# Performance work log

Hardware: AMD Instinct MI355X
Metric: run time of the kernel (lower is better)

The kernel has to match this reference:

```python
import jax, jax.numpy as jnp
import numpy as np
from jax import lax

B_SZ, C_IN, C_OUT, H_IM, W_IM = 2, 128, 128, 64, 64
N_STATE = 16
DT_RANK = 4  # ceil(128/32)


def _ln_cf(x, w, b, eps=1e-6):
    # channels_first LayerNorm over channel dim
    u = x.mean(1, keepdims=True)
    s = ((x - u) ** 2).mean(1, keepdims=True)
    return w[None, :, None, None] * (x - u) / jnp.sqrt(s + eps) + b[None, :, None, None]


def _bn_train(x, g, b, eps=1e-5):
    # BatchNorm2d in training mode (batch statistics, biased variance)
    m = x.mean((0, 2, 3), keepdims=True)
    v = ((x - m) ** 2).mean((0, 2, 3), keepdims=True)
    return g[None, :, None, None] * (x - m) / jnp.sqrt(v + eps) + b[None, :, None, None]


def _dwconv(x, w, b):
    y = lax.conv_general_dilated(x, w, (1, 1), 'SAME', feature_group_count=x.shape[1],
                                 dimension_numbers=('NCHW', 'OIHW', 'NCHW'))
    return y + b[None, :, None, None]


def _conv1x1(x, w, b):
    return jnp.einsum('oi,bihw->bohw', w, x) + b[None, :, None, None]


def _selective_scan(u, dt, A, Bm, Cm, D, delta_bias):
    # u, dt: [B,Ch,L]; A: [Ch,N]; Bm, Cm: [B,N,L]; D: [Ch]
    dt = jax.nn.softplus(dt + delta_bias[None, :, None])
    xs = (dt.transpose(2, 0, 1), u.transpose(2, 0, 1), Bm.transpose(2, 0, 1), Cm.transpose(2, 0, 1))
    h0 = jnp.zeros(u.shape[:2] + (A.shape[1],), u.dtype)

    def step(h, inp):
        dt_t, u_t, b_t, c_t = inp
        dA = jnp.exp(dt_t[..., None] * A)                        # [B,Ch,N]
        h = h * dA + (dt_t * u_t)[..., None] * b_t[:, None, :]   # [B,Ch,N]
        return h, jnp.einsum('bcn,bn->bc', h, c_t)

    _, ys = lax.scan(step, h0, xs)
    return ys.transpose(1, 2, 0) + u * D[None, :, None]


def _ssm_apply(u, Wx, bx, Wdt, bdt, Alog, D, r):
    # u: [B,Ch,L]. Replicates torch row-major .reshape of [(B L),D] -> [B,D,L].
    Bb, Ch, L = u.shape
    N = Alog.shape[1]
    x_flat = u.transpose(0, 2, 1).reshape(Bb * L, Ch)   # 'b c l -> (b l) c'
    x_dbl = x_flat @ Wx.T + bx
    dt = (x_dbl[:, :r] @ Wdt.T + bdt).reshape(Bb, Wdt.shape[0], L)
    Bm = x_dbl[:, r:r + N].reshape(Bb, N, L)
    Cm = x_dbl[:, r + N:].reshape(Bb, N, L)
    return _selective_scan(u, dt, -jnp.exp(Alog), Bm, Cm, D, bdt)


def _forward(x, ln_in_w, ln_in_b, inproj_w, inproj_b, ln_mamba_w, ln_mamba_b, convm_w, convm_b,
             convr_w, convr_b, ln_cat_w, ln_cat_b, xproj_f_w, xproj_f_b, dtproj_f_w, dtproj_f_b,
             Alog_f, D_f, xproj_b_w, xproj_b_b, dtproj_b_w, dtproj_b_b, Alog_b, D_b,
             xproj_u_w, xproj_u_b, dtproj_u_w, dtproj_u_b, Alog_u, D_u, gate1_w, gate1_b,
             bn_g, bn_b, gate2_w, gate2_b, outproj_w, outproj_b, outln_w, outln_b):
    Bb, C, H, W = x.shape
    L = H * W
    half = C // 2
    x = _ln_cf(x, ln_in_w, ln_in_b)
    xp = _conv1x1(x, inproj_w, inproj_b)
    x_mamba, x_res = xp[:, :C], xp[:, C:]
    x_mamba = _ln_cf(x_mamba, ln_mamba_w, ln_mamba_b)
    x_mamba = jax.nn.silu(_dwconv(x_mamba, convm_w, convm_b))
    x_res = jax.nn.silu(_dwconv(x_res, convr_w, convr_b))
    # forward scan on first half of channels
    xf = x_mamba[:, :half].reshape(Bb, half, L)
    yf = _ssm_apply(xf, xproj_f_w, xproj_f_b, dtproj_f_w, dtproj_f_b, Alog_f, D_f, DT_RANK).reshape(Bb, half, H, W)
    # backward scan on second half (flip H,W, scan, flip back)
    xb = x_mamba[:, half:][:, :, ::-1, ::-1]
    yb = _ssm_apply(xb.reshape(Bb, half, L), xproj_b_w, xproj_b_b, dtproj_b_w, dtproj_b_b,
                    Alog_b, D_b, DT_RANK).reshape(Bb, half, H, W)[:, :, ::-1, ::-1]
    concat = _ln_cf(jnp.concatenate([yf, yb], axis=1), ln_cat_w, ln_cat_b)
    # uncertainty-ordered scan on full x_mamba
    sig = jax.nn.sigmoid(x_mamba.mean(1, keepdims=True))
    unc = (-(sig * jnp.log(sig + 1e-6))).reshape(Bb, L)
    idx = jnp.argsort(-unc, axis=1)       # descending uncertainty
    inv = jnp.argsort(idx, axis=1)        # inverse permutation
    xs = jnp.take_along_axis(x_mamba.reshape(Bb, C, L), idx[:, None, :], axis=2)
    yu = _ssm_apply(xs, xproj_u_w, xproj_u_b, dtproj_u_w, dtproj_u_b, Alog_u, D_u, 2 * DT_RANK)
    yu = jnp.take_along_axis(yu, inv[:, None, :], axis=2).reshape(Bb, C, H, W)
    # gated fusion
    g = jax.nn.relu(_bn_train(_conv1x1(jnp.concatenate([concat, yu], 1), gate1_w, gate1_b), bn_g, bn_b))
    g = jax.nn.sigmoid(_conv1x1(g, gate2_w, gate2_b))
    fused = g * yu + (1.0 - g) * concat
    out = _conv1x1(jnp.concatenate([fused, x_res], 1), outproj_w, outproj_b)
    return _ln_cf(out, outln_w, outln_b)


def setup_inputs() -> dict:
    key = jax.random.key(0)
    ks = jax.random.split(key, 16)
    C, half, R, N = C_IN, C_IN // 2, DT_RANK, N_STATE
    rn = lambda k, shp, s=0.02: jax.random.normal(k, shp, jnp.float32) * s

    def inv_dt(k, n):
        dt = jnp.exp(jax.random.uniform(k, (n,)) * (np.log(0.1) - np.log(0.001)) + np.log(0.001))
        dt = jnp.maximum(dt, 1e-4)
        return dt + jnp.log(-jnp.expm1(-dt))

    std = R ** -0.5
    Alog_h = jnp.log(jnp.broadcast_to(jnp.arange(1, N + 1, dtype=jnp.float32), (half, N)))
    Alog_fl = jnp.log(jnp.broadcast_to(jnp.arange(1, N + 1, dtype=jnp.float32), (C, N)))
    return {
        'x': jax.random.normal(ks[0], (B_SZ, C, H_IM, W_IM), jnp.float32),
        'ln_in_w': jnp.ones(C), 'ln_in_b': jnp.zeros(C),
        'inproj_w': rn(ks[1], (2 * C, C)), 'inproj_b': jnp.zeros(2 * C),
        'ln_mamba_w': jnp.ones(C), 'ln_mamba_b': jnp.zeros(C),
        'convm_w': rn(ks[2], (C, 1, 3, 3), 0.1), 'convm_b': jnp.zeros(C),
        'convr_w': rn(ks[3], (C, 1, 3, 3), 0.1), 'convr_b': jnp.zeros(C),
        'ln_cat_w': jnp.ones(C), 'ln_cat_b': jnp.zeros(C),
        'xproj_f_w': rn(ks[4], (R + 2 * N, half)), 'xproj_f_b': jnp.zeros(R + 2 * N),
        'dtproj_f_w': jax.random.uniform(ks[5], (half, R), minval=-std, maxval=std),
        'dtproj_f_b': inv_dt(ks[6], half),
        'Alog_f': Alog_h, 'D_f': jnp.ones(half),
        'xproj_b_w': rn(ks[7], (R + 2 * N, half)), 'xproj_b_b': jnp.zeros(R + 2 * N),
        'dtproj_b_w': jax.random.uniform(ks[8], (half, R), minval=-std, maxval=std),
        'dtproj_b_b': inv_dt(ks[9], half),
        'Alog_b': Alog_h, 'D_b': jnp.ones(half),
        'xproj_u_w': rn(ks[10], (2 * R + 2 * N, C)), 'xproj_u_b': jnp.zeros(2 * R + 2 * N),
        'dtproj_u_w': jax.random.uniform(ks[11], (C, 2 * R), minval=-std, maxval=std),
        'dtproj_u_b': inv_dt(ks[12], C),
        'Alog_u': Alog_fl, 'D_u': jnp.ones(C),
        'gate1_w': rn(ks[13], (C, 2 * C)), 'gate1_b': jnp.zeros(C),
        'bn_g': jnp.ones(C), 'bn_b': jnp.zeros(C),
        'gate2_w': rn(ks[14], (C, C)), 'gate2_b': jnp.zeros(C),
        'outproj_w': rn(ks[15], (C_OUT, 2 * C)), 'outproj_b': jnp.zeros(C_OUT),
        'outln_w': jnp.ones(C_OUT), 'outln_b': jnp.zeros(C_OUT),
    }


def reference(x, ln_in_w, ln_in_b, inproj_w, inproj_b, ln_mamba_w, ln_mamba_b, convm_w, convm_b,
              convr_w, convr_b, ln_cat_w, ln_cat_b, xproj_f_w, xproj_f_b, dtproj_f_w, dtproj_f_b,
              Alog_f, D_f, xproj_b_w, xproj_b_b, dtproj_b_w, dtproj_b_b, Alog_b, D_b,
              xproj_u_w, xproj_u_b, dtproj_u_w, dtproj_u_b, Alog_u, D_u, gate1_w, gate1_b,
              bn_g, bn_b, gate2_w, gate2_b, outproj_w, outproj_b, outln_w, outln_b):
    return _forward(x, ln_in_w, ln_in_b, inproj_w, inproj_b, ln_mamba_w, ln_mamba_b, convm_w, convm_b,
                    convr_w, convr_b, ln_cat_w, ln_cat_b, xproj_f_w, xproj_f_b, dtproj_f_w, dtproj_f_b,
                    Alog_f, D_f, xproj_b_w, xproj_b_b, dtproj_b_w, dtproj_b_b, Alog_b, D_b,
                    xproj_u_w, xproj_u_b, dtproj_u_w, dtproj_u_b, Alog_u, D_u, gate1_w, gate1_b,
                    bn_g, bn_b, gate2_w, gate2_b, outproj_w, outproj_b, outln_w, outln_b)
```

## Files before the change

### kernel.cpp

```cpp
#include <hip/hip_runtime.h>
#include <cstdint>
#include <cstddef>

#define TPB 256

namespace {

constexpr int B_SZ = 2;
constexpr int C    = 128;
constexpr int HALF = 64;
constexpr int L    = 4096;
constexpr int N    = 16;
constexpr int HH   = 64;
constexpr int WW   = 64;

__device__ __forceinline__ float softplusf(float x) {
  return fmaxf(x, 0.f) + __logf(1.f + __expf(-fabsf(x)));
}
__device__ __forceinline__ float sigm(float x) { return 1.f / (1.f + __expf(-x)); }

__device__ __forceinline__ unsigned long long unc_key(float u, int i) {
  unsigned m = __float_as_uint(u);
  m = (m & 0x80000000u) ? ~m : (m | 0x80000000u);
  return ((unsigned long long)(~m) << 32) | (unsigned)i;
}

__global__ void k_pixstats(const float* __restrict__ X, int bsX, int Cn, float eps,
                           float* __restrict__ mean, float* __restrict__ rinv) {
  const int lp = threadIdx.x & 63;
  const int wv = threadIdx.x >> 6;
  const int p  = blockIdx.x * 64 + lp;
  const int b = p / L, l = p % L;
  const int Cq = Cn >> 2;
  const float* Xp = X + (size_t)b * bsX + l;
  float s = 0.f, s2 = 0.f;
#pragma unroll 8
  for (int i = 0; i < Cq; ++i) {
    float v = Xp[(size_t)(wv * Cq + i) * L];
    s += v; s2 += v * v;
  }
  __shared__ float r1[4][64], r2[4][64];
  r1[wv][lp] = s; r2[wv][lp] = s2;
  __syncthreads();
  if (wv == 0) {
    float st  = r1[0][lp] + r1[1][lp] + r1[2][lp] + r1[3][lp];
    float s2t = r2[0][lp] + r2[1][lp] + r2[2][lp] + r2[3][lp];
    float m = st / Cn;
    float var = s2t / Cn - m * m;
    mean[p] = m;
    rinv[p] = rsqrtf(var + eps);
  }
}

template <int O_PB>
__global__ void k_conv_ln(const float* __restrict__ X, int bsX,
                          const float* __restrict__ lnw, const float* __restrict__ lnb,
                          const float* __restrict__ W, const float* __restrict__ bias,
                          float* __restrict__ Y, int I, int O) {
  __shared__ float Wl[O_PB * 128];
  __shared__ float aw[128], ab[128];
  const int o0 = blockIdx.y * O_PB;
  const int b  = blockIdx.z;
  for (int t = threadIdx.x; t < O_PB * I; t += TPB) {
    int i = t / O_PB, k = t % O_PB;
    Wl[t] = W[(size_t)(o0 + k) * I + i];
  }
  for (int t = threadIdx.x; t < I; t += TPB) { aw[t] = lnw[t]; ab[t] = lnb[t]; }
  __syncthreads();
  const int l0 = blockIdx.x * (2 * TPB) + threadIdx.x;
  const int l1 = l0 + TPB;
  const float* X0 = X + (size_t)b * bsX + l0;
  const float* X1 = X + (size_t)b * bsX + l1;
  float s0 = 0.f, q0 = 0.f, s1 = 0.f, q1 = 0.f;
#pragma unroll 8
  for (int i = 0; i < I; ++i) {
    float v0 = X0[(size_t)i * L], v1 = X1[(size_t)i * L];
    s0 += v0; q0 += v0 * v0; s1 += v1; q1 += v1 * v1;
  }
  const float m0 = s0 / I, m1 = s1 / I;
  const float r0 = rsqrtf(q0 / I - m0 * m0 + 1e-6f);
  const float r1 = rsqrtf(q1 / I - m1 * m1 + 1e-6f);
  float acc0[O_PB], acc1[O_PB];
#pragma unroll
  for (int k = 0; k < O_PB; ++k) { acc0[k] = bias[o0 + k]; acc1[k] = acc0[k]; }
#pragma unroll 4
  for (int i = 0; i < I; ++i) {
    float xv0 = (X0[(size_t)i * L] - m0) * r0 * aw[i] + ab[i];
    float xv1 = (X1[(size_t)i * L] - m1) * r1 * aw[i] + ab[i];
#pragma unroll
    for (int k = 0; k < O_PB; ++k) {
      acc0[k] += Wl[i * O_PB + k] * xv0;
      acc1[k] += Wl[i * O_PB + k] * xv1;
    }
  }
#pragma unroll
  for (int k = 0; k < O_PB; ++k) {
    Y[((size_t)b * O + o0 + k) * L + l0] = acc0[k];
    Y[((size_t)b * O + o0 + k) * L + l1] = acc1[k];
  }
}

__global__ void k_dwconv_t(const float* __restrict__ xp,
                           const float* __restrict__ mean1, const float* __restrict__ rinv1,
                           const float* __restrict__ lnw, const float* __restrict__ lnb,
                           const float* __restrict__ Wm, const float* __restrict__ bm,
                           const float* __restrict__ Wr, const float* __restrict__ br,
                           float* __restrict__ xm, float* __restrict__ xr) {
  const int c = blockIdx.y;
  const int z = blockIdx.z;
  const int b = z & 1, mode = z >> 1;
  const int h0 = blockIdx.x * 4;
  __shared__ float T[6][66];
  const float* Xc = xp + ((size_t)b * 2 * C + (mode ? C + c : c)) * L;
  const float lw = mode ? 0.f : lnw[c];
  const float lb2 = mode ? 0.f : lnb[c];
  for (int t = threadIdx.x; t < 6 * 66; t += TPB) {
    int r = t / 66, cc = t % 66 - 1;
    int hh = h0 - 1 + r;
    float v = 0.f;
    if (hh >= 0 && hh < HH && cc >= 0 && cc < WW) {
      int li = hh * WW + cc;
      v = Xc[li];
      if (mode == 0) v = (v - mean1[b * L + li]) * rinv1[b * L + li] * lw + lb2;
    }
    T[r][t % 66] = v;
  }
  __syncthreads();
  const int hl = threadIdx.x >> 6, w = threadIdx.x & 63;
  const float* W9 = (mode ? Wr : Wm) + c * 9;
  float acc = mode ? br[c] : bm[c];
#pragma unroll
  for (int kh = 0; kh < 3; ++kh)
#pragma unroll
    for (int kw = 0; kw < 3; ++kw)
      acc += T[hl + kh][w + kw] * W9[kh * 3 + kw];
  const int l = (h0 + hl) * WW + w;
  float* Yp = mode ? xr : xm;
  Yp[((size_t)b * C + c) * L + l] = acc * sigm(acc);
}

__global__ void k_unc(const float* __restrict__ xm, float* __restrict__ unc,
                      float* __restrict__ bnsum, int* __restrict__ rankbuf) {
  if (blockIdx.x == 0) bnsum[threadIdx.x] = 0.f;
  const int gt = blockIdx.x * TPB + threadIdx.x;
  if (gt < B_SZ * L) rankbuf[gt] = 0;
  const int lp = threadIdx.x & 63;
  const int wv = threadIdx.x >> 6;
  const int p  = blockIdx.x * 64 + lp;
  const int b = p / L, l = p % L;
  const float* Xp = xm + (size_t)b * C * L + l;
  float s = 0.f;
#pragma unroll 8
  for (int i = 0; i < 32; ++i) s += Xp[(size_t)(wv * 32 + i) * L];
  __shared__ float r1[4][64];
  r1[wv][lp] = s;
  __syncthreads();
  if (wv == 0) {
    float st = r1[0][lp] + r1[1][lp] + r1[2][lp] + r1[3][lp];
    float sg = sigm(st / C);
    unc[p] = -(sg * __logf(sg + 1e-6f));
  }
}

__global__ void k_rank(const float* __restrict__ unc, int* __restrict__ rankbuf) {
  constexpr int JC = 512;
  __shared__ unsigned long long K[JC];
  const int b  = blockIdx.z;
  const int j0 = blockIdx.y * JC;
  const int i  = blockIdx.x * TPB + threadIdx.x;
  for (int t = threadIdx.x; t < JC; t += TPB)
    K[t] = unc_key(unc[b * L + j0 + t], j0 + t);
  __syncthreads();
  const unsigned long long my = unc_key(unc[b * L + i], i);
  int cnt = 0;
#pragma unroll 8
  for (int j = 0; j < JC; ++j) cnt += (K[j] < my) ? 1 : 0;
  atomicAdd(&rankbuf[b * L + i], cnt);
}

__global__ void k_scatgath(const float* __restrict__ xm, const int* __restrict__ rankbuf,
                           float* __restrict__ xs, int* __restrict__ inv) {
  int t = blockIdx.x * TPB + threadIdx.x;
  int l = t % L, c = (t / L) % C, b = t / (C * L);
  int r = rankbuf[b * L + l];
  xs[((size_t)b * C + c) * L + r] = xm[t];
  if (c == 0) inv[b * L + l] = r;
}

__global__ void k_unsort(const float* __restrict__ yus, const int* __restrict__ inv,
                         float* __restrict__ yu) {
  int t = blockIdx.x * TPB + threadIdx.x;
  int l = t % L, c = (t / L) % C, b = t / (C * L);
  yu[t] = yus[((size_t)b * C + c) * L + inv[b * L + l]];
}

__global__ void k_convx_all(const float* __restrict__ xm, const float* __restrict__ xs,
                            const float* __restrict__ Wf, const float* __restrict__ bf,
                            const float* __restrict__ Wb, const float* __restrict__ bb,
                            const float* __restrict__ Wu, const float* __restrict__ bu,
                            float* __restrict__ XDF, float* __restrict__ XDU) {
  const int z = blockIdx.z;
  const bool isU = z >= 4;
  const int I = isU ? 128 : 64;
  const int O = isU ? 40 : 36;
  const int o0 = blockIdx.y * 4;
  if (o0 >= O) return;
  int b, dir;
  const float *W, *bi;
  if (!isU) { dir = z >> 1; b = z & 1; W = dir ? Wb : Wf; bi = dir ? bb : bf; }
  else      { dir = 0; b = z - 4; W = Wu; bi = bu; }
  __shared__ float Wl[4 * 128];
  for (int t = threadIdx.x; t < 4 * I; t += TPB) {
    int i = t / 4, k = t % 4;
    Wl[t] = W[(size_t)(o0 + k) * I + i];
  }
  __syncthreads();
  const int l = blockIdx.x * TPB + threadIdx.x;
  const int ls = isU ? l : (dir ? (L - 1 - l) : l);
  const float* Xb = isU ? (xs + (size_t)b * C * L)
                        : (xm + ((size_t)b * C + dir * HALF) * L);
  float acc[4];
#pragma unroll
  for (int k = 0; k < 4; ++k) acc[k] = bi[o0 + k];
#pragma unroll 4
  for (int i = 0; i < I; ++i) {
    float xv = Xb[(size_t)i * L + ls];
#pragma unroll
    for (int k = 0; k < 4; ++k) acc[k] += Wl[i * 4 + k] * xv;
  }
  float* yp = isU ? (XDU + ((size_t)b * L + l) * 40 + o0)
                  : (XDF + ((size_t)z * L + l) * 36 + o0);
#pragma unroll
  for (int k = 0; k < 4; ++k) yp[k] = acc[k];
}

__global__ void k_bc_all(const float* __restrict__ xdblF, const float* __restrict__ xdblU,
                         float* __restrict__ BmTF, float* __restrict__ CmTF,
                         float* __restrict__ BmTU, float* __restrict__ CmTU) {
  const int z = blockIdx.z;
  const bool isU = z >= 4;
  const int RT = isU ? 8 : 4, OT = isU ? 40 : 36;
  const float* src = isU ? (xdblU + (size_t)(z - 4) * L * 40)
                         : (xdblF + (size_t)z * L * 36);
  float* BT = isU ? (BmTU + (size_t)(z - 4) * L * N) : (BmTF + (size_t)z * L * N);
  float* CT = isU ? (CmTU + (size_t)(z - 4) * L * N) : (CmTF + (size_t)z * L * N);
  const int n = blockIdx.y;
  const int l2 = blockIdx.x * TPB + threadIdx.x;
  int f2 = n * L + l2;
  int lb = f2 >> 4, cb = f2 & 15;
  const float* xr2 = src + (size_t)lb * OT + RT + cb;
  size_t ob = (size_t)l2 * N + n;
  BT[ob] = xr2[0];
  CT[ob] = xr2[N];
}

__global__ __launch_bounds__(1024) void
k_scan_all(const float* __restrict__ xdblF, const float* __restrict__ xdblU,
           const float* __restrict__ dtf_w, const float* __restrict__ dtf_b,
           const float* __restrict__ dtb_w, const float* __restrict__ dtb_b,
           const float* __restrict__ dtu_w, const float* __restrict__ dtu_b,
           const float* __restrict__ xm, const float* __restrict__ xs,
           const float* __restrict__ BmTF, const float* __restrict__ CmTF,
           const float* __restrict__ BmTU, const float* __restrict__ CmTU,
           const float* __restrict__ Alog_f, const float* __restrict__ Alog_b,
           const float* __restrict__ Alog_u,
           const float* __restrict__ D_f, const float* __restrict__ D_b,
           const float* __restrict__ D_u,
           float* __restrict__ yf, float* __restrict__ yb, float* __restrict__ yus) {
  const int blk = blockIdx.x;
  const int tid = threadIdx.x;
  const bool isU = blk >= 256;
  int CsT, RT, c, b, dir;
  const float *Wdt, *bdt, *Alog, *Dv, *xdbl, *BT, *CT, *Ub;
  float* Y;
  int OT;
  if (!isU) {
    CsT = 64; RT = 4; OT = 36;
    int zb = blk >> 6; c = blk & 63; dir = zb >> 1; b = zb & 1;
    Wdt = dir ? dtb_w : dtf_w; bdt = dir ? dtb_b : dtf_b;
    Alog = dir ? Alog_b : Alog_f; Dv = dir ? D_b : D_f;
    xdbl = xdblF + (size_t)zb * L * 36;
    BT = BmTF + (size_t)zb * L * N; CT = CmTF + (size_t)zb * L * N;
    Ub = xm + ((size_t)b * C + dir * HALF + c) * L;
    Y = (dir ? yb : yf) + ((size_t)b * HALF + c) * L;
  } else {
    CsT = 128; RT = 8; OT = 40;
    int blk2 = blk - 256; b = blk2 >> 7; c = blk2 & 127; dir = 0;
    Wdt = dtu_w; bdt = dtu_b; Alog = Alog_u; Dv = D_u;
    xdbl = xdblU + (size_t)b * L * 40;
    BT = BmTU + (size_t)b * L * N; CT = CmTU + (size_t)b * L * N;
    Ub = xs + ((size_t)b * C + c) * L;
    Y = yus + ((size_t)b * C + c) * L;
  }
  __shared__ float sW[1024];
  __shared__ float sb2[128];
  __shared__ float dtL[64][65];
  __shared__ float duL[64][65];
  __shared__ float SdL[64];
  __shared__ float sA[N][65], sH[N][65];
  for (int t = tid; t < CsT * RT; t += 1024) {
    int csrc = t / RT, r = t % RT;
    sW[r * CsT + csrc] = Wdt[t];
  }
  for (int t = tid; t < CsT; t += 1024) sb2[t] = bdt[t];
  __syncthreads();
  {
    const int chunk_d = tid >> 4;
    const int sq = (tid & 15) * 4;
    const int lsrc = isU ? (c * 32 + (chunk_d >> 1)) : (c * 64 + chunk_d);
    const float* xrp = xdbl + (size_t)lsrc * OT;
    float xr[8];
    for (int r = 0; r < RT; ++r) xr[r] = xrp[r];
    const float bcc = sb2[c];
    float dpart = 0.f;
#pragma unroll
    for (int j = 0; j < 4; ++j) {
      int s = sq + j;
      int csrc = isU ? (((chunk_d & 1) << 6) + s) : s;
      float acc = sb2[csrc] + bcc;
      for (int r = 0; r < RT; ++r) acc += sW[r * CsT + csrc] * xr[r];
      int l = (chunk_d << 6) + s;
      float d = softplusf(acc);
      float uv = Ub[isU ? l : (dir ? (L - 1 - l) : l)];
      dtL[chunk_d][s] = d;
      duL[chunk_d][s] = d * uv;
      dpart += d;
    }
    dpart += __shfl_xor(dpart, 1);
    dpart += __shfl_xor(dpart, 2);
    dpart += __shfl_xor(dpart, 4);
    dpart += __shfl_xor(dpart, 8);
    if ((tid & 15) == 0) SdL[chunk_d] = dpart;
  }
  __syncthreads();
  const int n = tid & 15;
  const int chunk = tid >> 4;
  const float a = -__expf(Alog[c * N + n]);
  const float* bp = BT + ((size_t)(chunk << 6)) * N + n;
  const float* cp = CT + ((size_t)(chunk << 6)) * N + n;
  float h = 0.f;
#pragma unroll 4
  for (int s = 0; s < 64; ++s) {
    float d = dtL[chunk][s];
    float du = duL[chunk][s];
    float bn = bp[(size_t)s * N];
    h = h * __expf(d * a) + du * bn;
  }
  sA[n][chunk] = __expf(a * SdL[chunk]);
  sH[n][chunk] = h;
  __syncthreads();
  {
    const int w = tid >> 6;
    const int k = tid & 63;
    float A = sA[w][k];
    float Bv = sH[w][k];
#pragma unroll
    for (int j = 1; j < 64; j <<= 1) {
      float pa = __shfl_up(A, j);
      float pb = __shfl_up(Bv, j);
      if (k >= j) { Bv = pb * A + Bv; A = pa * A; }
    }
    float hprev = __shfl_up(Bv, 1);
    sH[w][k] = (k == 0) ? 0.f : hprev;
  }
  __syncthreads();
  h = sH[n][chunk];
  const float Dc = Dv[c];
  float ybuf[4];
#pragma unroll 4
  for (int s = 0; s < 64; ++s) {
    float d = dtL[chunk][s];
    float du = duL[chunk][s];
    float bn = bp[(size_t)s * N];
    float cn = cp[(size_t)s * N];
    h = h * __expf(d * a) + du * bn;
    float p = h * cn;
    p += __shfl_xor(p, 1);
    p += __shfl_xor(p, 2);
    p += __shfl_xor(p, 4);
    p += __shfl_xor(p, 8);
    if ((s & 15) == n) {
      float uv = du / fmaxf(d, 1e-30f);
      ybuf[s >> 4] = p + uv * Dc;
    }
  }
  float* Yp = Y + (chunk << 6);
#pragma unroll
  for (int q = 0; q < 4; ++q) Yp[16 * q + n] = ybuf[q];
}

template <int O_PB>
__global__ void k_gate1(const float* __restrict__ yf, const float* __restrict__ yb,
                        const float* __restrict__ lncw, const float* __restrict__ lncb,
                        const float* __restrict__ yu,
                        const float* __restrict__ W, const float* __restrict__ bias,
                        float* __restrict__ g1,
                        float* __restrict__ st2m, float* __restrict__ st2r,
                        float* __restrict__ bnsum) {
  __shared__ float Wl[O_PB * 256];
  __shared__ float cw[128], cb2[128];
  __shared__ float part[2][O_PB][4];
  const int o0 = blockIdx.y * O_PB;
  const int b  = blockIdx.z;
  for (int t = threadIdx.x; t < O_PB * 256; t += TPB) {
    int i = t / O_PB, k = t % O_PB;
    Wl[t] = W[(size_t)(o0 + k) * 256 + i];
  }
  for (int t = threadIdx.x; t < 128; t += TPB) { cw[t] = lncw[t]; cb2[t] = lncb[t]; }
  __syncthreads();
  const int l = blockIdx.x * TPB + threadIdx.x;
  const float* f0 = yf + (size_t)b * HALF * L + l;
  const float* b0 = yb + (size_t)b * HALF * L + (L - 1 - l);
  const float* u0 = yu + (size_t)b * C * L + l;
  float s = 0.f, s2 = 0.f;
#pragma unroll 8
  for (int i = 0; i < 64; ++i) { float v = f0[(size_t)i * L]; s += v; s2 += v * v; }
#pragma unroll 8
  for (int i = 0; i < 64; ++i) { float v = b0[(size_t)i * L]; s += v; s2 += v * v; }
  const float m = s / C;
  const float r = rsqrtf(s2 / C - m * m + 1e-6f);
  if (blockIdx.y == 0) { st2m[b * L + l] = m; st2r[b * L + l] = r; }
  float acc[O_PB];
#pragma unroll
  for (int k = 0; k < O_PB; ++k) acc[k] = bias[o0 + k];
#pragma unroll 4
  for (int i = 0; i < 64; ++i) {
    float cv = (f0[(size_t)i * L] - m) * r * cw[i] + cb2[i];
#pragma unroll
    for (int k = 0; k < O_PB; ++k) acc[k] += Wl[i * O_PB + k] * cv;
  }
#pragma unroll 4
  for (int i = 0; i < 64; ++i) {
    float cv = (b0[(size_t)i * L] - m) * r * cw[64 + i] + cb2[64 + i];
#pragma unroll
    for (int k = 0; k < O_PB; ++k) acc[k] += Wl[(64 + i) * O_PB + k] * cv;
  }
#pragma unroll 4
  for (int i = 0; i < 128; ++i) {
    float xv = u0[(size_t)i * L];
#pragma unroll
    for (int k = 0; k < O_PB; ++k) acc[k] += Wl[(128 + i) * O_PB + k] * xv;
  }
#pragma unroll
  for (int k = 0; k < O_PB; ++k)
    g1[((size_t)b * C + o0 + k) * L + l] = acc[k];
  const int wv = threadIdx.x >> 6, lnn = threadIdx.x & 63;
#pragma unroll
  for (int k = 0; k < O_PB; ++k) {
    float v = acc[k];
    v += __shfl_xor(v, 1);  v += __shfl_xor(v, 2);  v += __shfl_xor(v, 4);
    v += __shfl_xor(v, 8);  v += __shfl_xor(v, 16); v += __shfl_xor(v, 32);
    if (lnn == 0) part[0][k][wv] = v;
    float q = acc[k] * acc[k];
    q += __shfl_xor(q, 1);  q += __shfl_xor(q, 2);  q += __shfl_xor(q, 4);
    q += __shfl_xor(q, 8);  q += __shfl_xor(q, 16); q += __shfl_xor(q, 32);
    if (lnn == 0) part[1][k][wv] = q;
  }
  __syncthreads();
  if (threadIdx.x < 2 * O_PB) {
    int which = threadIdx.x >= O_PB, k = threadIdx.x % O_PB;
    float v = part[which][k][0] + part[which][k][1] + part[which][k][2] + part[which][k][3];
    atomicAdd(&bnsum[which * 128 + o0 + k], v);
  }
}

template <int O_PB>
__global__ void k_gate2_fuse(const float* __restrict__ g1,
                             const float* __restrict__ bnsum,
                             const float* __restrict__ bn_g, const float* __restrict__ bn_b,
                             const float* __restrict__ W, const float* __restrict__ bias,
                             const float* __restrict__ yu,
                             const float* __restrict__ yf, const float* __restrict__ yb,
                             const float* __restrict__ mean2, const float* __restrict__ rinv2,
                             const float* __restrict__ lncw, const float* __restrict__ lncb,
                             float* __restrict__ fused) {
  __shared__ float Wl[O_PB * 128];
  __shared__ float sc[128], sh[128];
  __shared__ float cwo[O_PB], cbo[O_PB];
  const int o0 = blockIdx.y * O_PB;
  const int b  = blockIdx.z;
  for (int t = threadIdx.x; t < O_PB * 128; t += TPB) {
    int i = t / O_PB, k = t % O_PB;
    Wl[t] = W[(size_t)(o0 + k) * 128 + i];
  }
  for (int t = threadIdx.x; t < 128; t += TPB) {
    float sv = bnsum[t], qv = bnsum[128 + t];
    float mean = sv / (B_SZ * L);
    float var  = qv / (B_SZ * L) - mean * mean;
    float scv = bn_g[t] * rsqrtf(var + 1e-5f);
    sc[t] = scv;
    sh[t] = bn_b[t] - mean * scv;
  }
  if (threadIdx.x < O_PB) {
    cwo[threadIdx.x] = lncw[o0 + threadIdx.x];
    cbo[threadIdx.x] = lncb[o0 + threadIdx.x];
  }
  __syncthreads();
  const int l = blockIdx.x * TPB + threadIdx.x;
  const float m = mean2[b * L + l], r = rinv2[b * L + l];
  const float* Xb = g1 + (size_t)b * C * L + l;
  float acc[O_PB];
#pragma unroll
  for (int k = 0; k < O_PB; ++k) acc[k] = bias[o0 + k];
#pragma unroll 4
  for (int i = 0; i < 128; ++i) {
    float v = fmaxf(Xb[(size_t)i * L] * sc[i] + sh[i], 0.f);
#pragma unroll
    for (int k = 0; k < O_PB; ++k) acc[k] += Wl[i * O_PB + k] * v;
  }
#pragma unroll
  for (int k = 0; k < O_PB; ++k) {
    int o = o0 + k;
    float g = sigm(acc[k]);
    float yuv = yu[((size_t)b * C + o) * L + l];
    float yv = (o < 64) ? yf[((size_t)b * HALF + o) * L + l]
                        : yb[((size_t)b * HALF + (o - 64)) * L + (L - 1 - l)];
    float cv = (yv - m) * r * cwo[k] + cbo[k];
    fused[((size_t)b * C + o) * L + l] = g * yuv + (1.f - g) * cv;
  }
}

template <int O_PB>
__global__ void k_conv1x1_cat2(const float* __restrict__ X1, const float* __restrict__ X2,
                               const float* __restrict__ W, const float* __restrict__ bias,
                               float* __restrict__ Y, int O) {
  __shared__ float Wl[O_PB * 256];
  const int o0 = blockIdx.y * O_PB;
  const int b  = blockIdx.z;
  for (int t = threadIdx.x; t < O_PB * 256; t += TPB) {
    int i = t / O_PB, k = t % O_PB;
    Wl[t] = W[(size_t)(o0 + k) * 256 + i];
  }
  __syncthreads();
  const int l = blockIdx.x * TPB + threadIdx.x;
  const float* Xb1 = X1 + (size_t)b * C * L + l;
  const float* Xb2 = X2 + (size_t)b * C * L + l;
  float acc[O_PB];
#pragma unroll
  for (int k = 0; k < O_PB; ++k) acc[k] = bias[o0 + k];
#pragma unroll 4
  for (int i = 0; i < 128; ++i) {
    float xv = Xb1[(size_t)i * L];
#pragma unroll
    for (int k = 0; k < O_PB; ++k) acc[k] += Wl[i * O_PB + k] * xv;
  }
#pragma unroll 4
  for (int i = 0; i < 128; ++i) {
    float xv = Xb2[(size_t)i * L];
#pragma unroll
    for (int k = 0; k < O_PB; ++k) acc[k] += Wl[(128 + i) * O_PB + k] * xv;
  }
#pragma unroll
  for (int k = 0; k < O_PB; ++k)
    Y[((size_t)b * O + o0 + k) * L + l] = acc[k];
}

__global__ void k_ln_cf(const float* __restrict__ X,
                        const float* __restrict__ w, const float* __restrict__ bchan,
                        float* __restrict__ Y) {
  const int lp = threadIdx.x & 63;
  const int wv = threadIdx.x >> 6;
  const int p  = blockIdx.x * 64 + lp;
  const int b = p / L, l = p % L;
  const float* Xp = X + (size_t)b * C * L + l;
  float s = 0.f, s2 = 0.f;
#pragma unroll 8
  for (int i = 0; i < 32; ++i) {
    float v = Xp[(size_t)(wv * 32 + i) * L];
    s += v; s2 += v * v;
  }
  __shared__ float r1[4][64], r2[4][64];
  r1[wv][lp] = s; r2[wv][lp] = s2;
  __syncthreads();
  float st  = r1[0][lp] + r1[1][lp] + r1[2][lp] + r1[3][lp];
  float s2t = r2[0][lp] + r2[1][lp] + r2[2][lp] + r2[3][lp];
  float mean = st / C;
  float rinv = rsqrtf(s2t / C - mean * mean + 1e-6f);
  float* Yp = Y + (size_t)b * C * L + l;
#pragma unroll 8
  for (int i = 0; i < 32; ++i) {
    int c = wv * 32 + i;
    float v = Xp[(size_t)c * L];
    Yp[(size_t)c * L] = w[c] * (v - mean) * rinv + bchan[c];
  }
}

}

extern "C" void kernel_launch(void* const* d_in, const int* in_sizes, int n_in,
                              void* d_out, int out_size, void* d_ws, size_t ws_size,
                              hipStream_t stream) {
  const float* x         = (const float*)d_in[0];
  const float* ln_in_w   = (const float*)d_in[1];
  const float* ln_in_b   = (const float*)d_in[2];
  const float* inproj_w  = (const float*)d_in[3];
  const float* inproj_b  = (const float*)d_in[4];
  const float* ln_m_w    = (const float*)d_in[5];
  const float* ln_m_b    = (const float*)d_in[6];
  const float* convm_w   = (const float*)d_in[7];
  const float* convm_b   = (const float*)d_in[8];
  const float* convr_w   = (const float*)d_in[9];
  const float* convr_b   = (const float*)d_in[10];
  const float* ln_cat_w  = (const float*)d_in[11];
  const float* ln_cat_b  = (const float*)d_in[12];
  const float* xpf_w     = (const float*)d_in[13];
  const float* xpf_b     = (const float*)d_in[14];
  const float* dtf_w     = (const float*)d_in[15];
  const float* dtf_b     = (const float*)d_in[16];
  const float* Alog_f    = (const float*)d_in[17];
  const float* D_f       = (const float*)d_in[18];
  const float* xpb_w     = (const float*)d_in[19];
  const float* xpb_b     = (const float*)d_in[20];
  const float* dtb_w     = (const float*)d_in[21];
  const float* dtb_b     = (const float*)d_in[22];
  const float* Alog_b    = (const float*)d_in[23];
  const float* D_b       = (const float*)d_in[24];
  const float* xpu_w     = (const float*)d_in[25];
  const float* xpu_b     = (const float*)d_in[26];
  const float* dtu_w     = (const float*)d_in[27];
  const float* dtu_b     = (const float*)d_in[28];
  const float* Alog_u    = (const float*)d_in[29];
  const float* D_u       = (const float*)d_in[30];
  const float* gate1_w   = (const float*)d_in[31];
  const float* gate1_b   = (const float*)d_in[32];
  const float* bn_g      = (const float*)d_in[33];
  const float* bn_b      = (const float*)d_in[34];
  const float* gate2_w   = (const float*)d_in[35];
  const float* gate2_b   = (const float*)d_in[36];
  const float* outproj_w = (const float*)d_in[37];
  const float* outproj_b = (const float*)d_in[38];
  const float* outln_w   = (const float*)d_in[39];
  const float* outln_b   = (const float*)d_in[40];

  float* ws = (float*)d_ws;
  size_t off = 0;
  auto alloc = [&](size_t n) { float* p = ws + off; off += n; return p; };

  const size_t BL = (size_t)B_SZ * L;
  float* xp    = alloc((size_t)B_SZ * 2 * C * L);
  float* st1m  = alloc(BL);
  float* st1r  = alloc(BL);
  float* xm    = alloc((size_t)B_SZ * C * L);
  float* xr    = alloc((size_t)B_SZ * C * L);
  float* unc   = alloc(BL);
  int*   rank  = (int*)alloc(BL);
  int*   inv   = (int*)alloc(BL);
  float* xs    = alloc((size_t)B_SZ * C * L);
  float* xdblF = alloc((size_t)4 * L * 36);
  float* BmTF  = alloc((size_t)4 * L * N);
  float* CmTF  = alloc((size_t)4 * L * N);
  float* xdblU = alloc((size_t)2 * L * 40);
  float* BmTU  = alloc((size_t)2 * L * N);
  float* CmTU  = alloc((size_t)2 * L * N);
  float* yf    = alloc((size_t)B_SZ * HALF * L);
  float* yb    = alloc((size_t)B_SZ * HALF * L);
  float* yus   = alloc((size_t)B_SZ * C * L);
  float* yu    = alloc((size_t)B_SZ * C * L);
  float* st2m  = alloc(BL);
  float* st2r  = alloc(BL);
  float* g1    = alloc((size_t)B_SZ * C * L);
  float* bnsum = alloc(256);
  float* fused = alloc((size_t)B_SZ * C * L);
  float* outp  = alloc((size_t)B_SZ * C * L);
  (void)ws_size; (void)in_sizes; (void)n_in; (void)out_size;

  const int pixB = B_SZ * L / 64;
  const int elemB = B_SZ * C * L / TPB;

  k_conv_ln<16><<<dim3(L / (2 * TPB), 16, B_SZ), TPB, 0, stream>>>(
      x, C * L, ln_in_w, ln_in_b, inproj_w, inproj_b, xp, 128, 256);
  k_pixstats<<<pixB, TPB, 0, stream>>>(xp, 2 * C * L, C, 1e-6f, st1m, st1r);
  k_dwconv_t<<<dim3(HH / 4, C, 2 * B_SZ), TPB, 0, stream>>>(
      xp, st1m, st1r, ln_m_w, ln_m_b, convm_w, convm_b, convr_w, convr_b, xm, xr);
  k_unc<<<pixB, TPB, 0, stream>>>(xm, unc, bnsum, rank);
  k_rank<<<dim3(L / TPB, 8, B_SZ), TPB, 0, stream>>>(unc, rank);
  k_scatgath<<<elemB, TPB, 0, stream>>>(xm, rank, xs, inv);
  k_convx_all<<<dim3(L / TPB, 10, 6), TPB, 0, stream>>>(
      xm, xs, xpf_w, xpf_b, xpb_w, xpb_b, xpu_w, xpu_b, xdblF, xdblU);
  k_bc_all<<<dim3(L / TPB, N, 6), TPB, 0, stream>>>(
      xdblF, xdblU, BmTF, CmTF, BmTU, CmTU);
  k_scan_all<<<512, 1024, 0, stream>>>(
      xdblF, xdblU, dtf_w, dtf_b, dtb_w, dtb_b, dtu_w, dtu_b,
      xm, xs, BmTF, CmTF, BmTU, CmTU,
      Alog_f, Alog_b, Alog_u, D_f, D_b, D_u, yf, yb, yus);
  k_unsort<<<elemB, TPB, 0, stream>>>(yus, inv, yu);
  k_gate1<8><<<dim3(L / TPB, 16, B_SZ), TPB, 0, stream>>>(
      yf, yb, ln_cat_w, ln_cat_b, yu, gate1_w, gate1_b, g1, st2m, st2r, bnsum);
  k_gate2_fuse<8><<<dim3(L / TPB, 16, B_SZ), TPB, 0, stream>>>(
      g1, bnsum, bn_g, bn_b, gate2_w, gate2_b, yu, yf, yb, st2m, st2r,
      ln_cat_w, ln_cat_b, fused);
  k_conv1x1_cat2<8><<<dim3(L / TPB, 16, B_SZ), TPB, 0, stream>>>(
      fused, xr, outproj_w, outproj_b, outp, 128);
  k_ln_cf<<<pixB, TPB, 0, stream>>>(outp, outln_w, outln_b, (float*)d_out);
}
```

Before: 358.4 us.

## Fuse LN stats into in-proj conv and unsort into scan epilogue

Removes the separate pixel-statistics pass by accumulating per-pixel sum and sum of squares with atomics in the in-projection kernel. Halves the outputs per block and doubles the grid. Removes the unsort kernel by having the scan write unsorted outputs through an inverse index, and replaces the scan's precomputed dt*u and dt-sum with per-step products. Zeroing moves to one memset. The trade-offs are atomic traffic, scattered scan stores, and a few extra multiplies in the scan loop.

New measurement: 341.8 us (median of 2 runs). -4.6%, faster.

```diff
diff --git a/kernel.cpp b/kernel.cpp
--- a/kernel.cpp
+++ b/kernel.cpp
@@ -25,38 +25,12 @@
   return ((unsigned long long)(~m) << 32) | (unsigned)i;
 }
 
-__global__ void k_pixstats(const float* __restrict__ X, int bsX, int Cn, float eps,
-                           float* __restrict__ mean, float* __restrict__ rinv) {
-  const int lp = threadIdx.x & 63;
-  const int wv = threadIdx.x >> 6;
-  const int p  = blockIdx.x * 64 + lp;
-  const int b = p / L, l = p % L;
-  const int Cq = Cn >> 2;
-  const float* Xp = X + (size_t)b * bsX + l;
-  float s = 0.f, s2 = 0.f;
-#pragma unroll 8
-  for (int i = 0; i < Cq; ++i) {
-    float v = Xp[(size_t)(wv * Cq + i) * L];
-    s += v; s2 += v * v;
-  }
-  __shared__ float r1[4][64], r2[4][64];
-  r1[wv][lp] = s; r2[wv][lp] = s2;
-  __syncthreads();
-  if (wv == 0) {
-    float st  = r1[0][lp] + r1[1][lp] + r1[2][lp] + r1[3][lp];
-    float s2t = r2[0][lp] + r2[1][lp] + r2[2][lp] + r2[3][lp];
-    float m = st / Cn;
-    float var = s2t / Cn - m * m;
-    mean[p] = m;
-    rinv[p] = rsqrtf(var + eps);
-  }
-}
-
-template <int O_PB>
 __global__ void k_conv_ln(const float* __restrict__ X, int bsX,
                           const float* __restrict__ lnw, const float* __restrict__ lnb,
                           const float* __restrict__ W, const float* __restrict__ bias,
-                          float* __restrict__ Y, int I, int O) {
+                          float* __restrict__ Y, int I, int O,
+                          float* __restrict__ st1s, float* __restrict__ st1q) {
+  constexpr int O_PB = 8;
   __shared__ float Wl[O_PB * 128];
   __shared__ float aw[128], ab[128];
   const int o0 = blockIdx.y * O_PB;
@@ -98,10 +72,22 @@
     Y[((size_t)b * O + o0 + k) * L + l0] = acc0[k];
     Y[((size_t)b * O + o0 + k) * L + l1] = acc1[k];
   }
+  if (o0 < 128) {
+    float ss0 = 0.f, qq0 = 0.f, ss1 = 0.f, qq1 = 0.f;
+#pragma unroll
+    for (int k = 0; k < O_PB; ++k) {
+      ss0 += acc0[k]; qq0 += acc0[k] * acc0[k];
+      ss1 += acc1[k]; qq1 += acc1[k] * acc1[k];
+    }
+    atomicAdd(&st1s[b * L + l0], ss0);
+    atomicAdd(&st1q[b * L + l0], qq0);
+    atomicAdd(&st1s[b * L + l1], ss1);
+    atomicAdd(&st1q[b * L + l1], qq1);
+  }
 }
 
 __global__ void k_dwconv_t(const float* __restrict__ xp,
-                           const float* __restrict__ mean1, const float* __restrict__ rinv1,
+                           const float* __restrict__ st1s, const float* __restrict__ st1q,
                            const float* __restrict__ lnw, const float* __restrict__ lnb,
                            const float* __restrict__ Wm, const float* __restrict__ bm,
                            const float* __restrict__ Wr, const float* __restrict__ br,
@@ -121,7 +107,12 @@
     if (hh >= 0 && hh < HH && cc >= 0 && cc < WW) {
       int li = hh * WW + cc;
       v = Xc[li];
-      if (mode == 0) v = (v - mean1[b * L + li]) * rinv1[b * L + li] * lw + lb2;
+      if (mode == 0) {
+        float sv = st1s[b * L + li], qv = st1q[b * L + li];
+        float m = sv * (1.f / 128.f);
+        float rr = rsqrtf(qv * (1.f / 128.f) - m * m + 1e-6f);
+        v = (v - m) * rr * lw + lb2;
+      }
     }
     T[r][t % 66] = v;
   }
@@ -139,11 +130,7 @@
   Yp[((size_t)b * C + c) * L + l] = acc * sigm(acc);
 }
 
-__global__ void k_unc(const float* __restrict__ xm, float* __restrict__ unc,
-                      float* __restrict__ bnsum, int* __restrict__ rankbuf) {
-  if (blockIdx.x == 0) bnsum[threadIdx.x] = 0.f;
-  const int gt = blockIdx.x * TPB + threadIdx.x;
-  if (gt < B_SZ * L) rankbuf[gt] = 0;
+__global__ void k_unc(const float* __restrict__ xm, float* __restrict__ unc) {
   const int lp = threadIdx.x & 63;
   const int wv = threadIdx.x >> 6;
   const int p  = blockIdx.x * 64 + lp;
@@ -179,19 +166,13 @@
 }
 
 __global__ void k_scatgath(const float* __restrict__ xm, const int* __restrict__ rankbuf,
-                           float* __restrict__ xs, int* __restrict__ inv) {
+                           float* __restrict__ xs, int* __restrict__ inv,
+                           int* __restrict__ idx) {
   int t = blockIdx.x * TPB + threadIdx.x;
   int l = t % L, c = (t / L) % C, b = t / (C * L);
   int r = rankbuf[b * L + l];
   xs[((size_t)b * C + c) * L + r] = xm[t];
-  if (c == 0) inv[b * L + l] = r;
-}
-
-__global__ void k_unsort(const float* __restrict__ yus, const int* __restrict__ inv,
-                         float* __restrict__ yu) {
-  int t = blockIdx.x * TPB + threadIdx.x;
-  int l = t % L, c = (t / L) % C, b = t / (C * L);
-  yu[t] = yus[((size_t)b * C + c) * L + inv[b * L + l]];
+  if (c == 0) { inv[b * L + l] = r; idx[b * L + r] = l; }
 }
 
 __global__ void k_convx_all(const float* __restrict__ xm, const float* __restrict__ xs,
@@ -260,18 +241,20 @@
            const float* __restrict__ dtb_w, const float* __restrict__ dtb_b,
            const float* __restrict__ dtu_w, const float* __restrict__ dtu_b,
            const float* __restrict__ xm, const float* __restrict__ xs,
+           const int* __restrict__ idx,
            const float* __restrict__ BmTF, const float* __restrict__ CmTF,
            const float* __restrict__ BmTU, const float* __restrict__ CmTU,
            const float* __restrict__ Alog_f, const float* __restrict__ Alog_b,
            const float* __restrict__ Alog_u,
            const float* __restrict__ D_f, const float* __restrict__ D_b,
            const float* __restrict__ D_u,
-           float* __restrict__ yf, float* __restrict__ yb, float* __restrict__ yus) {
+           float* __restrict__ yf, float* __restrict__ yb, float* __restrict__ yu) {
   const int blk = blockIdx.x;
   const int tid = threadIdx.x;
   const bool isU = blk >= 256;
   int CsT, RT, c, b, dir;
   const float *Wdt, *bdt, *Alog, *Dv, *xdbl, *BT, *CT, *Ub;
+  const int* idxb = nullptr;
   float* Y;
   int OT;
   if (!isU) {
@@ -290,13 +273,13 @@
     xdbl = xdblU + (size_t)b * L * 40;
     BT = BmTU + (size_t)b * L * N; CT = CmTU + (size_t)b * L * N;
     Ub = xs + ((size_t)b * C + c) * L;
-    Y = yus + ((size_t)b * C + c) * L;
+    idxb = idx + b * L;
+    Y = yu + ((size_t)b * C + c) * L;
   }
   __shared__ float sW[1024];
   __shared__ float sb2[128];
   __shared__ float dtL[64][65];
-  __shared__ float duL[64][65];
-  __shared__ float SdL[64];
+  __shared__ float uL[64][65];
   __shared__ float sA[N][65], sH[N][65];
   for (int t = tid; t < CsT * RT; t += 1024) {
     int csrc = t / RT, r = t % RT;
@@ -312,7 +295,6 @@
     float xr[8];
     for (int r = 0; r < RT; ++r) xr[r] = xrp[r];
     const float bcc = sb2[c];
-    float dpart = 0.f;
 #pragma unroll
     for (int j = 0; j < 4; ++j) {
       int s = sq + j;
@@ -320,17 +302,9 @@
       float acc = sb2[csrc] + bcc;
       for (int r = 0; r < RT; ++r) acc += sW[r * CsT + csrc] * xr[r];
       int l = (chunk_d << 6) + s;
-      float d = softplusf(acc);
-      float uv = Ub[isU ? l : (dir ? (L - 1 - l) : l)];
-      dtL[chunk_d][s] = d;
-      duL[chunk_d][s] = d * uv;
-      dpart += d;
+      dtL[chunk_d][s] = softplusf(acc);
+      uL[chunk_d][s] = Ub[isU ? l : (dir ? (L - 1 - l) : l)];
     }
-    dpart += __shfl_xor(dpart, 1);
-    dpart += __shfl_xor(dpart, 2);
-    dpart += __shfl_xor(dpart, 4);
-    dpart += __shfl_xor(dpart, 8);
-    if ((tid & 15) == 0) SdL[chunk_d] = dpart;
   }
   __syncthreads();
   const int n = tid & 15;
@@ -338,16 +312,17 @@
   const float a = -__expf(Alog[c * N + n]);
   const float* bp = BT + ((size_t)(chunk << 6)) * N + n;
   const float* cp = CT + ((size_t)(chunk << 6)) * N + n;
-  float h = 0.f;
+  float ap = 1.f, h = 0.f;
 #pragma unroll 4
   for (int s = 0; s < 64; ++s) {
     float d = dtL[chunk][s];
-    float du = duL[chunk][s];
+    float uv = uL[chunk][s];
     float bn = bp[(size_t)s * N];
-    h = h * __expf(d * a) + du * bn;
-  }
-  sA[n][chunk] = __expf(a * SdL[chunk]);
-  sH[n][chunk] = h;
+    float dA = __expf(d * a);
+    ap *= dA;
+    h = h * dA + d * uv * bn;
+  }
+  sA[n][chunk] = ap; sH[n][chunk] = h;
   __syncthreads();
   {
     const int w = tid >> 6;
@@ -370,23 +345,27 @@
 #pragma unroll 4
   for (int s = 0; s < 64; ++s) {
     float d = dtL[chunk][s];
-    float du = duL[chunk][s];
+    float uv = uL[chunk][s];
     float bn = bp[(size_t)s * N];
     float cn = cp[(size_t)s * N];
-    h = h * __expf(d * a) + du * bn;
+    float dA = __expf(d * a);
+    h = h * dA + d * uv * bn;
     float p = h * cn;
     p += __shfl_xor(p, 1);
     p += __shfl_xor(p, 2);
     p += __shfl_xor(p, 4);
     p += __shfl_xor(p, 8);
-    if ((s & 15) == n) {
-      float uv = du / fmaxf(d, 1e-30f);
-      ybuf[s >> 4] = p + uv * Dc;
-    }
-  }
-  float* Yp = Y + (chunk << 6);
-#pragma unroll
-  for (int q = 0; q < 4; ++q) Yp[16 * q + n] = ybuf[q];
+    if ((s & 15) == n) ybuf[s >> 4] = p + uv * Dc;
+  }
+  if (!isU) {
+    float* Yp = Y + (chunk << 6);
+#pragma unroll
+    for (int q = 0; q < 4; ++q) Yp[16 * q + n] = ybuf[q];
+  } else {
+    const int s0 = chunk << 6;
+#pragma unroll
+    for (int q = 0; q < 4; ++q) Y[idxb[s0 + 16 * q + n]] = ybuf[q];
+  }
 }
 
 template <int O_PB>
@@ -637,14 +616,18 @@
   auto alloc = [&](size_t n) { float* p = ws + off; off += n; return p; };
 
   const size_t BL = (size_t)B_SZ * L;
+  float* st1s  = alloc(BL);
+  float* st1q  = alloc(BL);
+  int*   rank  = (int*)alloc(BL);
+  float* bnsum = alloc(256);
+  const size_t zeroBytes = (3 * BL + 256) * sizeof(float);
+
   float* xp    = alloc((size_t)B_SZ * 2 * C * L);
-  float* st1m  = alloc(BL);
-  float* st1r  = alloc(BL);
   float* xm    = alloc((size_t)B_SZ * C * L);
   float* xr    = alloc((size_t)B_SZ * C * L);
   float* unc   = alloc(BL);
-  int*   rank  = (int*)alloc(BL);
   int*   inv   = (int*)alloc(BL);
+  int*   idx   = (int*)alloc(BL);
   float* xs    = alloc((size_t)B_SZ * C * L);
   float* xdblF = alloc((size_t)4 * L * 36);
   float* BmTF  = alloc((size_t)4 * L * N);
@@ -654,12 +637,10 @@
   float* CmTU  = alloc((size_t)2 * L * N);
   float* yf    = alloc((size_t)B_SZ * HALF * L);
   float* yb    = alloc((size_t)B_SZ * HALF * L);
-  float* yus   = alloc((size_t)B_SZ * C * L);
   float* yu    = alloc((size_t)B_SZ * C * L);
   float* st2m  = alloc(BL);
   float* st2r  = alloc(BL);
   float* g1    = alloc((size_t)B_SZ * C * L);
-  float* bnsum = alloc(256);
   float* fused = alloc((size_t)B_SZ * C * L);
   float* outp  = alloc((size_t)B_SZ * C * L);
   (void)ws_size; (void)in_sizes; (void)n_in; (void)out_size;
@@ -667,23 +648,22 @@
   const int pixB = B_SZ * L / 64;
   const int elemB = B_SZ * C * L / TPB;
 
-  k_conv_ln<16><<<dim3(L / (2 * TPB), 16, B_SZ), TPB, 0, stream>>>(
-      x, C * L, ln_in_w, ln_in_b, inproj_w, inproj_b, xp, 128, 256);
-  k_pixstats<<<pixB, TPB, 0, stream>>>(xp, 2 * C * L, C, 1e-6f, st1m, st1r);
+  hipMemsetAsync(st1s, 0, zeroBytes, stream);
+  k_conv_ln<<<dim3(L / (2 * TPB), 32, B_SZ), TPB, 0, stream>>>(
+      x, C * L, ln_in_w, ln_in_b, inproj_w, inproj_b, xp, 128, 256, st1s, st1q);
   k_dwconv_t<<<dim3(HH / 4, C, 2 * B_SZ), TPB, 0, stream>>>(
-      xp, st1m, st1r, ln_m_w, ln_m_b, convm_w, convm_b, convr_w, convr_b, xm, xr);
-  k_unc<<<pixB, TPB, 0, stream>>>(xm, unc, bnsum, rank);
+      xp, st1s, st1q, ln_m_w, ln_m_b, convm_w, convm_b, convr_w, convr_b, xm, xr);
+  k_unc<<<pixB, TPB, 0, stream>>>(xm, unc);
   k_rank<<<dim3(L / TPB, 8, B_SZ), TPB, 0, stream>>>(unc, rank);
-  k_scatgath<<<elemB, TPB, 0, stream>>>(xm, rank, xs, inv);
+  k_scatgath<<<elemB, TPB, 0, stream>>>(xm, rank, xs, inv, idx);
   k_convx_all<<<dim3(L / TPB, 10, 6), TPB, 0, stream>>>(
       xm, xs, xpf_w, xpf_b, xpb_w, xpb_b, xpu_w, xpu_b, xdblF, xdblU);
   k_bc_all<<<dim3(L / TPB, N, 6), TPB, 0, stream>>>(
       xdblF, xdblU, BmTF, CmTF, BmTU, CmTU);
   k_scan_all<<<512, 1024, 0, stream>>>(
       xdblF, xdblU, dtf_w, dtf_b, dtb_w, dtb_b, dtu_w, dtu_b,
-      xm, xs, BmTF, CmTF, BmTU, CmTU,
-      Alog_f, Alog_b, Alog_u, D_f, D_b, D_u, yf, yb, yus);
-  k_unsort<<<elemB, TPB, 0, stream>>>(yus, inv, yu);
+      xm, xs, idx, BmTF, CmTF, BmTU, CmTU,
+      Alog_f, Alog_b, Alog_u, D_f, D_b, D_u, yf, yb, yu);
   k_gate1<8><<<dim3(L / TPB, 16, B_SZ), TPB, 0, stream>>>(
       yf, yb, ln_cat_w, ln_cat_b, yu, gate1_w, gate1_b, g1, st2m, st2r, bnsum);
   k_gate2_fuse<8><<<dim3(L / TPB, 16, B_SZ), TPB, 0, stream>>>(
```
